# Optimization experiments

Measured on AMD Instinct MI355X. Metric: run time of the kernel, lower is better.

The kernel has to match this reference:

```python
import jax, jax.numpy as jnp
import numpy as np

P = 7    # pool size (hard-coded in module)
DS = 16  # downsample rate


def _hat_int(t):
    # antiderivative of the bilinear hat kernel max(0, 1-|t|)
    t = jnp.clip(t, -1.0, 1.0)
    return jnp.where(t < 0, 0.5 * (t + 1.0) ** 2, 1.0 - 0.5 * (1.0 - t) ** 2)


def _axis_weights(lo, hi, size):
    # Exact per-pixel integration weights for PrRoIPool along one axis.
    # lo, hi: [R] scaled roi coords. Returns W [R,P,size], bin width [R].
    bw = (hi - lo) / P
    starts = lo[:, None] + bw[:, None] * jnp.arange(P, dtype=lo.dtype)  # [R,P]
    ends = starts + bw[:, None]
    idx = jnp.arange(size, dtype=lo.dtype)
    W = _hat_int(ends[:, :, None] - idx) - _hat_int(starts[:, :, None] - idx)
    return W, bw


def prroi_pool(feat, rois):
    # Precise RoI pooling: exact integral of the bilinearly-interpolated feature
    # over each bin (separable -> two small matmuls). feat [C,H,W], rois [R,4].
    C, H, Wd = feat.shape
    s = 1.0 / DS
    Wx, bw = _axis_weights(rois[:, 0] * s, rois[:, 2] * s, Wd)
    Wy, bh = _axis_weights(rois[:, 1] * s, rois[:, 3] * s, H)
    pooled = jnp.einsum('chw,rph,rqw->rcpq', feat, Wy, Wx)  # [R,C,P,P]
    area = jnp.maximum(bw * bh, 1e-8)
    return pooled / area[:, None, None, None]


def intersection_map(box1, box2):
    # Fractional coverage of each PxP bin of box2's grid by box1 -> [N,1,P,P]
    bw = (box2[:, 2] - box2[:, 0]) / P
    bh = (box2[:, 3] - box2[:, 1]) / P
    gx0 = box2[:, 0, None] + bw[:, None] * jnp.arange(P)
    gy0 = box2[:, 1, None] + bh[:, None] * jnp.arange(P)
    ox = jnp.clip(jnp.minimum(gx0 + bw[:, None], box1[:, 2, None]) - jnp.maximum(gx0, box1[:, 0, None]), 0.0)
    oy = jnp.clip(jnp.minimum(gy0 + bh[:, None], box1[:, 3, None]) - jnp.maximum(gy0, box1[:, 1, None]), 0.0)
    frac = oy[:, :, None] * ox[:, None, :] / jnp.maximum(bw * bh, 1e-8)[:, None, None]
    return frac[:, None]


def conv1x1(x, W, b):
    # 1x1 conv as a channel matmul; x [...,C,H,W], W [D,C], b [D]
    return jnp.einsum('...chw,dc->...dhw', x, W) + b[:, None, None]


def setup_inputs() -> dict:
    key = jax.random.key(0)
    ks = jax.random.split(key, 12)
    B, C, Hf, Wf, n = 8, 256, 32, 32, 16
    D1 = D2 = 256
    inp = jax.random.normal(ks[0], (B, C, Hf, Wf), dtype=jnp.float32)
    N = B * n
    xy1 = jax.random.uniform(ks[1], (N, 2), dtype=jnp.float32) * 380.0
    wh = 40.0 + jax.random.uniform(ks[2], (N, 2), dtype=jnp.float32) * 90.0
    objects = jnp.concatenate([xy1, xy1 + wh], axis=-1)  # valid boxes inside 512x512
    objects_length = jnp.full((B,), n, dtype=jnp.int32)

    def kaiming(k, shape, fan_in):
        return jax.random.normal(k, shape, dtype=jnp.float32) * np.float32(np.sqrt(2.0 / fan_in))

    rin = C // 2 * 3 + 2 * D1
    return {
        'input': inp, 'objects': objects, 'objects_length': objects_length,
        'Wc': kaiming(ks[3], (C, C), C), 'bc': jnp.zeros((C,), jnp.float32),
        'Wr': kaiming(ks[4], (C // 2 * 3, C), C), 'br': jnp.zeros((C // 2 * 3,), jnp.float32),
        'Wof': kaiming(ks[5], (D1, 2 * C), 2 * C), 'bof': jnp.zeros((D1,), jnp.float32),
        'Wrf': kaiming(ks[6], (D2, rin), rin), 'brf': jnp.zeros((D2,), jnp.float32),
        'Wofc': kaiming(ks[7], (D1, D1 * P * P), D1 * P * P), 'bofc': jnp.zeros((D1,), jnp.float32),
        'Wrfc': kaiming(ks[8], (D2, D2 * P * P), D2 * P * P), 'brfc': jnp.zeros((D2,), jnp.float32),
    }


def reference(input, objects, objects_length, Wc, bc, Wr, br, Wof, bof, Wrf, brf, Wofc, bofc, Wrfc, brfc):
    B, C, H, Wd = input.shape
    n = objects.shape[0] // B  # uniform object count per image
    boxes = objects.reshape(B, n, 4)
    ctx_all = conv1x1(input, Wc, bc)           # [B,C,H,W]
    rel_all = conv1x1(input, Wr, br)           # [B,3C/2,H,W]
    img_box = jnp.array([0.0, 0.0, Wd * DS, H * DS], dtype=input.dtype)
    sub_id = jnp.repeat(jnp.arange(n), n)
    obj_id = jnp.tile(jnp.arange(n), n)

    def per_image(feat, ctx, rel, box):
        # context pooled over the full-image box is identical for all objects
        ctx_pool = prroi_pool(ctx, img_box[None])[0]                    # [C,P,P]
        x_c, y_c = jnp.split(ctx_pool, 2, axis=0)
        box_imap = jax.lax.stop_gradient(
            intersection_map(box, jnp.broadcast_to(img_box, (n, 4))))  # [n,1,P,P]
        obj_pool = prroi_pool(feat, box)                                # [n,C,P,P]
        obj_in = jnp.concatenate([
            obj_pool,
            jnp.broadcast_to(x_c, (n,) + x_c.shape),
            y_c[None] * box_imap], axis=1)                              # [n,2C,P,P]
        obj_feat = conv1x1(obj_in, Wof, bof)                            # [n,D1,P,P]

        sub_box, ob_box = box[sub_id], box[obj_id]                      # [n*n,4]
        union = jax.lax.stop_gradient(jnp.concatenate(
            [jnp.minimum(sub_box[:, :2], ob_box[:, :2]),
             jnp.maximum(sub_box[:, 2:], ob_box[:, 2:])], axis=-1))
        sub_imap = jax.lax.stop_gradient(intersection_map(sub_box, union))
        obj_imap = jax.lax.stop_gradient(intersection_map(ob_box, union))
        rel_pool = prroi_pool(rel, union)                               # [n*n,3C/2,P,P]
        xr, yr, zr = jnp.split(rel_pool, 3, axis=1)
        rel_in = jnp.concatenate([
            obj_feat[sub_id], obj_feat[obj_id],
            xr, yr * sub_imap, zr * obj_imap], axis=1)                  # [n*n,2D1+3C/2,P,P]
        rel_feat = conv1x1(rel_in, Wrf, brf)                            # [n*n,D2,P,P]

        o = jax.nn.relu(obj_feat).reshape(n, -1) @ Wofc.T + bofc
        o = o / jnp.linalg.norm(o, axis=-1, keepdims=True)
        r = jax.nn.relu(rel_feat).reshape(n * n, -1) @ Wrfc.T + brfc
        r = r / jnp.linalg.norm(r, axis=-1, keepdims=True)
        return o, r.reshape(n, n, -1)

    obj_out, rel_out = jax.vmap(per_image)(input, ctx_all, rel_all, boxes)
    return obj_out, rel_out
```

## Files before the change

### kernel.cpp

```cpp
#include <hip/hip_runtime.h>
#include <hip/hip_bf16.h>


#define Bimg 8
#define Cch 256
#define HW 1024
#define CREL 384
#define CCAT 640
#define KFC 12544
#define STS 236

typedef __hip_bfloat16 bf16;
typedef __attribute__((ext_vector_type(8))) short short8;
typedef __attribute__((ext_vector_type(4))) short short4_t;
typedef __attribute__((ext_vector_type(4))) float f32x4;

__device__ __forceinline__ float hat_int(float t) {
    t = fminf(1.f, fmaxf(-1.f, t));
    return (t < 0.f) ? 0.5f * (t + 1.f) * (t + 1.f) : 1.f - 0.5f * (1.f - t) * (1.f - t);
}
__device__ __forceinline__ float b2f(short s) {
    return __uint_as_float(((unsigned)(unsigned short)s) << 16);
}
__device__ __forceinline__ unsigned pack2bf(float a, float b) {
    bf16 ha = __float2bfloat16(a), hb = __float2bfloat16(b);
    return ((unsigned)(unsigned short)(*(short*)&hb) << 16) | (unsigned short)(*(short*)&ha);
}

__global__ void prep_k(const float* __restrict__ Wc, const float* __restrict__ bc,
                       const float* __restrict__ Wr, const float* __restrict__ br,
                       bf16* __restrict__ Wcat, float* __restrict__ bcat,
                       const float* __restrict__ Wof, bf16* __restrict__ wof16,
                       const float* __restrict__ Wrf, bf16* __restrict__ wasao16,
                       bf16* __restrict__ wrfxyz16) {
    int bid = blockIdx.x, tid = threadIdx.x;
    if (bid < 640) {
        int t = bid * 256 + tid;
        int d = t >> 8, c = t & 255;
        Wcat[t] = __float2bfloat16((d < 256) ? Wc[d * 256 + c] : Wr[(d - 256) * 256 + c]);
        if (t < CCAT) bcat[t] = (t < 256) ? bc[t] : br[t - 256];
    } else if (bid < 1152) {
        int t = (bid - 640) * 256 + tid;
        wof16[t] = __float2bfloat16(Wof[t]);
    } else if (bid < 1664) {
        int t = (bid - 1152) * 256 + tid;
        int m = t >> 8, k = t & 255;
        wasao16[t] = __float2bfloat16((m < 256) ? Wrf[m * 896 + k] : Wrf[(m - 256) * 896 + 256 + k]);
    } else {
        int t = (bid - 1664) * 256 + tid;
        int d = t / 384, k = t - d * 384;
        wrfxyz16[t] = __float2bfloat16(Wrf[d * 896 + 512 + k]);
    }
}
__global__ __launch_bounds__(256) void wfc_pack_k(const float* __restrict__ W, bf16* __restrict__ dst) {
    __shared__ float ld[64 * 50];
    int dout = blockIdx.y, d0 = blockIdx.x * 64;
    int tid = threadIdx.x;
    for (int e = tid; e < 64 * 49; e += 256) {
        int di = e / 49, pq = e - di * 49;
        ld[di * 50 + pq] = W[(size_t)dout * KFC + (d0 + di) * 49 + pq];
    }
    __syncthreads();
    for (int e = tid; e < 64 * 49; e += 256) {
        int pq = e >> 6, di = e & 63;
        if (pq < 49)
            dst[(size_t)dout * KFC + pq * 256 + d0 + di] = __float2bfloat16(ld[di * 50 + pq]);
    }
}

__global__ void axisw_k(const float* __restrict__ objects,
                        float* __restrict__ orec, float* __restrict__ urec,
                        float* __restrict__ crec, float* __restrict__ bimap) {
    int bid = blockIdx.x;
    float b0, b1, b2, b3;
    float* rec;
    const float *sbp = nullptr, *obp = nullptr;
    if (bid < 128) {
        b0 = objects[bid * 4]; b1 = objects[bid * 4 + 1];
        b2 = objects[bid * 4 + 2]; b3 = objects[bid * 4 + 3];
        rec = orec + (size_t)bid * 128;
    } else if (bid < 2176) {
        int u = bid - 128;
        int img = u >> 8, pair = u & 255, i = pair >> 4, j = pair & 15;
        sbp = objects + (img * 16 + i) * 4;
        obp = objects + (img * 16 + j) * 4;
        b0 = fminf(sbp[0], obp[0]); b1 = fminf(sbp[1], obp[1]);
        b2 = fmaxf(sbp[2], obp[2]); b3 = fmaxf(sbp[3], obp[3]);
        rec = urec + (size_t)(u) * 224;
    } else {
        b0 = 0.f; b1 = 0.f; b2 = 512.f; b3 = 512.f;
        rec = crec;
    }
    const float sc = 0.0625f;
    float lox = b0 * sc, bwx = (b2 * sc - lox) * (1.f / 7.f);
    float loy = b1 * sc, bwy = (b3 * sc - loy) * (1.f / 7.f);
    float ia = 1.f / fmaxf(bwx * bwy, 1e-8f);
    int tid = threadIdx.x;
    if (tid < 56) {
        int p = tid >> 3, k = tid & 7;
        {
            float st = loy + bwy * p, en = st + bwy;
            int h0 = min(max((int)floorf(st) - 1, 0), 24);
            rec[tid] = hat_int(en - (float)(h0 + k)) - hat_int(st - (float)(h0 + k));
            if (k == 0) ((int*)rec)[119 + p] = h0;
        }
        {
            float st = lox + bwx * p, en = st + bwx;
            int w0 = min(max((int)floorf(st) - 1, 0), 24);
            rec[56 + tid] = ia * (hat_int(en - (float)(w0 + k)) - hat_int(st - (float)(w0 + k)));
            if (k == 0) ((int*)rec)[112 + p] = w0;
        }
    }
    if (tid < 49) {
        int p = tid / 7, q = tid - p * 7;
        if (bid < 128) {
            float bw = 512.f / 7.f, bh = 512.f / 7.f;
            float gx0 = bw * q, gy0 = bh * p;
            float ox = fmaxf(fminf(gx0 + bw, b2) - fmaxf(gx0, b0), 0.f);
            float oy = fmaxf(fminf(gy0 + bh, b3) - fmaxf(gy0, b1), 0.f);
            bimap[bid * 49 + tid] = oy * ox / fmaxf(bw * bh, 1e-8f);
        } else if (bid < 2176) {
            float bw = (b2 - b0) * (1.f / 7.f), bh = (b3 - b1) * (1.f / 7.f);
            float gx0 = b0 + bw * q, gy0 = b1 + bh * p;
            float inv = 1.f / fmaxf(bw * bh, 1e-8f);
            float oxs = fmaxf(fminf(gx0 + bw, sbp[2]) - fmaxf(gx0, sbp[0]), 0.f);
            float oys = fmaxf(fminf(gy0 + bh, sbp[3]) - fmaxf(gy0, sbp[1]), 0.f);
            rec[126 + tid] = oys * oxs * inv;
            float oxo = fmaxf(fminf(gx0 + bw, obp[2]) - fmaxf(gx0, obp[0]), 0.f);
            float oyo = fmaxf(fminf(gy0 + bh, obp[3]) - fmaxf(gy0, obp[1]), 0.f);
            rec[175 + tid] = oyo * oxo * inv;
        }
    }
}

__global__ __launch_bounds__(256) void int_t_k(const float* __restrict__ input, bf16* __restrict__ intp) {
    __shared__ float st[64][65];
    int hw0 = blockIdx.x * 64, c0 = blockIdx.y * 64, b = blockIdx.z;
    int tid = threadIdx.x;
#pragma unroll
    for (int i = 0; i < 16; i++) {
        int e = tid + i * 256;
        int c = e >> 6, hw = e & 63;
        st[c][hw] = input[(size_t)b * 262144 + (size_t)(c0 + c) * 1024 + hw0 + hw];
    }
    __syncthreads();
#pragma unroll
    for (int i = 0; i < 16; i++) {
        int e = tid + i * 256;
        int hw = e >> 6, c = e & 63;
        intp[((size_t)b * 1024 + hw0 + hw) * 256 + c0 + c] = __float2bfloat16(st[c][hw]);
    }
}

__global__ __launch_bounds__(256) void mfma_gemm_k(
    const bf16* __restrict__ A, int lda,
    const bf16* __restrict__ BT, int ldbt, long zB,
    int Ktiles, int splitk, int mode,
    float* __restrict__ Cf, int Mtot, int Ntot,
    const float* __restrict__ bias,
    const bf16* __restrict__ ASAOT, int bimg0,
    bf16* __restrict__ Ct, int ldct, long zC, bf16* __restrict__ Ct2) {
    __shared__ float tr[32 * 132];
    const int tid = threadIdx.x;
    const int m0 = blockIdx.y * 128, n0 = blockIdx.x * 128;
    int z = blockIdx.z;
    int kz = 0, bimg = bimg0;
    if (mode == 1) { BT += (size_t)z * zB; Ct += (size_t)z * zC; bimg = bimg0 + z; }
    else kz = z;
    const int tp = (Ktiles + splitk - 1) / splitk;
    const int kt0 = kz * tp;
    const int kt1 = min(Ktiles, kt0 + tp);
    const int lane = tid & 63, wid = tid >> 6;
    const int wm = (wid >> 1) * 64, wn = (wid & 1) * 64;
    const int lrow = lane & 15, lk = (lane >> 4) * 8;
    f32x4 acc[4][4];
#pragma unroll
    for (int i = 0; i < 4; i++)
#pragma unroll
        for (int j = 0; j < 4; j++) acc[i][j] = (f32x4){0.f, 0.f, 0.f, 0.f};
    const bf16* pA = A + (size_t)(m0 + wm + lrow) * lda + lk;
    const bf16* pB = BT + (size_t)(n0 + wn + lrow) * ldbt + lk;
    short8 a_c[4], b_c[4];
    if (kt0 < kt1) {
#pragma unroll
        for (int f = 0; f < 4; f++) {
            a_c[f] = *(const short8*)(pA + (size_t)f * 16 * lda + (size_t)kt0 * 32);
            b_c[f] = *(const short8*)(pB + (size_t)f * 16 * ldbt + (size_t)kt0 * 32);
        }
    }
    for (int kt = kt0; kt < kt1; kt++) {
        short8 a_n[4], b_n[4];
        if (kt + 1 < kt1) {
#pragma unroll
            for (int f = 0; f < 4; f++) {
                a_n[f] = *(const short8*)(pA + (size_t)f * 16 * lda + (size_t)(kt + 1) * 32);
                b_n[f] = *(const short8*)(pB + (size_t)f * 16 * ldbt + (size_t)(kt + 1) * 32);
            }
        }
#pragma unroll
        for (int i = 0; i < 4; i++)
#pragma unroll
            for (int j = 0; j < 4; j++)
                acc[i][j] = __builtin_amdgcn_mfma_f32_16x16x32_bf16(a_c[i], b_c[j], acc[i][j], 0, 0, 0);
#pragma unroll
        for (int f = 0; f < 4; f++) { a_c[f] = a_n[f]; b_c[f] = b_n[f]; }
    }
    const int rbase = (lane >> 4) * 4, cf = lane & 15;
    if (mode == 5) {
#pragma unroll
        for (int i = 0; i < 4; i++)
#pragma unroll
            for (int reg = 0; reg < 4; reg++) {
                int m = m0 + wm + i * 16 + rbase + reg;
                float bv = bias[m];
#pragma unroll
                for (int j = 0; j < 4; j++) {
                    int n = n0 + wn + j * 16 + cf;
                    Ct[(size_t)m * ldct + n] = __float2bfloat16(acc[i][j][reg] + bv);
                }
            }
        return;
    }
#pragma unroll 1
    for (int ci = 0; ci < 4; ci++) {
        __syncthreads();
        if ((wid & 1) == (ci >> 1)) {
            int jj0 = (ci & 1) * 2;
#pragma unroll
            for (int jj = jj0; jj < jj0 + 2; jj++)
#pragma unroll
                for (int i = 0; i < 4; i++)
#pragma unroll
                    for (int reg = 0; reg < 4; reg++) {
                        int nl = (wn + jj * 16 + cf) - 32 * ci;
                        int ml = wm + i * 16 + rbase + reg;
                        tr[nl * 132 + ml] = acc[i][jj][reg];
                    }
        }
        __syncthreads();
        if (mode == 2) {
            float* P = Cf + (size_t)kz * Mtot * Ntot;
            for (int e = tid; e < 1024; e += 256) {
                int nl = e >> 5, mq = (e & 31) * 4;
                int n = n0 + 32 * ci + nl;
                *(f32x4*)&P[(size_t)n * Mtot + m0 + mq] = *(f32x4*)&tr[nl * 132 + mq];
            }
        } else if (mode == 3 || mode == 6) {
            for (int e = tid; e < 2048; e += 256) {
                int nl = e >> 6, mq = (e & 63) * 2;
                int n = n0 + 32 * ci + nl;
                int m = m0 + mq;
                float v0 = tr[nl * 132 + mq] + (bias ? bias[m] : 0.f);
                float v1 = tr[nl * 132 + mq + 1] + (bias ? bias[m + 1] : 0.f);
                *(unsigned*)&Ct[(size_t)n * ldct + m] = pack2bf(v0, v1);
                if (mode == 6) {
                    int r = n / 49, pq = n - r * 49;
                    *(unsigned*)&Ct2[(size_t)r * KFC + pq * 256 + m] =
                        pack2bf(fmaxf(v0, 0.f), fmaxf(v1, 0.f));
                }
            }
        } else {
            for (int e = tid; e < 2048; e += 256) {
                int nl = e >> 6, mq = (e & 63) * 2;
                int n = n0 + 32 * ci + nl;
                int m = m0 + mq;
                int r = n / 49, pq = n - r * 49;
                int ii = r >> 4, jj2 = r & 15;
                size_t abase = ((size_t)bimg * 784 + ii * 49 + pq) * 512;
                size_t obase = ((size_t)bimg * 784 + jj2 * 49 + pq) * 512 + 256;
                float v0 = tr[nl * 132 + mq] + bias[m]
                         + b2f(*(const short*)&ASAOT[abase + m])
                         + b2f(*(const short*)&ASAOT[obase + m]);
                float v1 = tr[nl * 132 + mq + 1] + bias[m + 1]
                         + b2f(*(const short*)&ASAOT[abase + m + 1])
                         + b2f(*(const short*)&ASAOT[obase + m + 1]);
                *(unsigned*)&Ct[(size_t)r * KFC + pq * 256 + m] =
                    pack2bf(fmaxf(v0, 0.f), fmaxf(v1, 0.f));
            }
        }
    }
}

__global__ __launch_bounds__(256) void objpool_k(
    const float* __restrict__ input, const float* __restrict__ orec,
    bf16* __restrict__ objint) {
    int cg = blockIdx.x;
    int b = blockIdx.y;
    __shared__ float sF[8192];
    __shared__ float sT[2][1888];
    __shared__ float wb[2][128];
    int tid = threadIdx.x;
    const float* feat = input + (size_t)b * (Cch * HW) + (size_t)cg * 8 * HW;
    for (int e4 = tid; e4 < 2048; e4 += 256)
        *(f32x4*)&sF[e4 * 4] = *(const f32x4*)&feat[e4 * 4];
    const float* rb = orec + (size_t)b * 16 * 128;
    if (tid < 126) wb[0][tid] = rb[tid];
    int t1v = tid + 256;
    int c0 = tid / 56, r0 = tid - c0 * 56, p0 = r0 >> 3, w40 = r0 & 7;
    int c1 = t1v / 56, r1 = t1v - c1 * 56, p1 = r1 >> 3, w41 = r1 & 7;
    bool has1 = (t1v < 448);
    int sf0 = c0 * 1024 + w40 * 4, st0 = c0 * STS + p0 * 32 + w40 * 4;
    int sf1 = c1 * 1024 + w41 * 4, st1 = c1 * STS + p1 * 32 + w41 * 4;
    int xpq0 = tid >> 3, xc = tid & 7;
    int xp0 = xpq0 / 7, xq0 = xpq0 - xp0 * 7;
    int xpq1 = xpq0 + 32;
    int xp1 = xpq1 / 7, xq1 = xpq1 - xp1 * 7;
    bool xv1 = (xpq1 < 49);
    __syncthreads();
    for (int r2 = 0; r2 < 16; r2++) {
        const float* wc_ = wb[r2 & 1];
        float* stbuf = sT[r2 & 1];
        float pre;
        bool pf = (r2 < 15) && (tid < 126);
        if (pf) pre = rb[(r2 + 1) * 128 + tid];
        {
            int h0 = ((const int*)wc_)[119 + p0];
            const f32x4* f = (const f32x4*)&sF[sf0 + h0 * 32];
            f32x4 wya = *(const f32x4*)&wc_[p0 * 8];
            f32x4 wyb = *(const f32x4*)&wc_[p0 * 8 + 4];
            f32x4 a = f[0] * wya[0] + f[8] * wya[1] + f[16] * wya[2] + f[24] * wya[3]
                    + f[32] * wyb[0] + f[40] * wyb[1] + f[48] * wyb[2] + f[56] * wyb[3];
            *(f32x4*)&stbuf[st0] = a;
        }
        if (has1) {
            int h0 = ((const int*)wc_)[119 + p1];
            const f32x4* f = (const f32x4*)&sF[sf1 + h0 * 32];
            f32x4 wya = *(const f32x4*)&wc_[p1 * 8];
            f32x4 wyb = *(const f32x4*)&wc_[p1 * 8 + 4];
            f32x4 a = f[0] * wya[0] + f[8] * wya[1] + f[16] * wya[2] + f[24] * wya[3]
                    + f[32] * wyb[0] + f[40] * wyb[1] + f[48] * wyb[2] + f[56] * wyb[3];
            *(f32x4*)&stbuf[st1] = a;
        }
        f32x4 xwa0 = *(const f32x4*)&wc_[56 + xq0 * 8];
        f32x4 xwb0 = *(const f32x4*)&wc_[56 + xq0 * 8 + 4];
        int w0i0 = ((const int*)wc_)[112 + xq0];
        f32x4 xwa1 = {0, 0, 0, 0}, xwb1 = {0, 0, 0, 0};
        int w0i1 = 0;
        if (xv1) {
            xwa1 = *(const f32x4*)&wc_[56 + xq1 * 8];
            xwb1 = *(const f32x4*)&wc_[56 + xq1 * 8 + 4];
            w0i1 = ((const int*)wc_)[112 + xq1];
        }
        if (pf) wb[1 - (r2 & 1)][tid] = pre;
        __syncthreads();
        {
            bf16* orow = objint + ((size_t)b * 784 + (size_t)r2 * 49) * 512 + cg * 8 + xc;
            {
                const float* t = &stbuf[xc * STS + xp0 * 32 + w0i0];
                float s = t[0] * xwa0[0] + t[1] * xwa0[1] + t[2] * xwa0[2] + t[3] * xwa0[3]
                        + t[4] * xwb0[0] + t[5] * xwb0[1] + t[6] * xwb0[2] + t[7] * xwb0[3];
                orow[(size_t)xpq0 * 512] = __float2bfloat16(s);
            }
            if (xv1) {
                const float* t = &stbuf[xc * STS + xp1 * 32 + w0i1];
                float s = t[0] * xwa1[0] + t[1] * xwa1[1] + t[2] * xwa1[2] + t[3] * xwa1[3]
                        + t[4] * xwb1[0] + t[5] * xwb1[1] + t[6] * xwb1[2] + t[7] * xwb1[3];
                orow[(size_t)xpq1 * 512] = __float2bfloat16(s);
            }
        }
    }
}

__global__ __launch_bounds__(256) void ctxobjin_k(
    const bf16* __restrict__ ctxrelb, const float* __restrict__ crec,
    const float* __restrict__ bimap, bf16* __restrict__ objint) {
    int cg = blockIdx.x;
    int b = blockIdx.y;
    __shared__ float sF[8192];
    __shared__ float sT[1888];
    __shared__ float wc_[128];
    __shared__ float sBI[784];
    int tid = threadIdx.x;
    for (int e4 = tid; e4 < 2048; e4 += 256) {
        short4_t v = *(const short4_t*)&ctxrelb[(size_t)(cg * 8 + (e4 >> 8)) * 8192 + b * 1024 + (e4 & 255) * 4];
        f32x4 fv = {b2f(v[0]), b2f(v[1]), b2f(v[2]), b2f(v[3])};
        *(f32x4*)&sF[e4 * 4] = fv;
    }
    if (tid < 126) wc_[tid] = crec[tid];
    for (int e = tid; e < 784; e += 256) sBI[e] = bimap[b * 784 + e];
    __syncthreads();
    for (int tt = tid; tt < 448; tt += 256) {
        int c = tt / 56, r = tt - c * 56, p = r >> 3, w4 = r & 7;
        int h0 = ((const int*)wc_)[119 + p];
        const f32x4* f = (const f32x4*)&sF[c * 1024 + w4 * 4 + h0 * 32];
        f32x4 wya = *(const f32x4*)&wc_[p * 8];
        f32x4 wyb = *(const f32x4*)&wc_[p * 8 + 4];
        f32x4 a = f[0] * wya[0] + f[8] * wya[1] + f[16] * wya[2] + f[24] * wya[3]
                + f[32] * wyb[0] + f[40] * wyb[1] + f[48] * wyb[2] + f[56] * wyb[3];
        *(f32x4*)&sT[c * STS + p * 32 + w4 * 4] = a;
    }
    __syncthreads();
    bool scale = (cg >= 16);
    for (int e = tid; e < 392; e += 256) {
        int pq = e >> 3, c = e & 7;
        int p = pq / 7, q = pq - p * 7;
        int w0i = ((const int*)wc_)[112 + q];
        const float* t = &sT[c * STS + p * 32 + w0i];
        const f32x4* wx4 = (const f32x4*)&wc_[56 + q * 8];
        f32x4 a = wx4[0], b2 = wx4[1];
        float s = t[0] * a[0] + t[1] * a[1] + t[2] * a[2] + t[3] * a[3]
                + t[4] * b2[0] + t[5] * b2[1] + t[6] * b2[2] + t[7] * b2[3];
        int j = cg * 8 + c;
        bf16* orow = objint + ((size_t)b * 784 + pq) * 512 + 256 + j;
#pragma unroll
        for (int r = 0; r < 16; r++) {
            float m = scale ? sBI[r * 49 + pq] : 1.f;
            orow[(size_t)r * 49 * 512] = __float2bfloat16(s * m);
        }
    }
}

__global__ __launch_bounds__(256) void relpool_k(
    const bf16* __restrict__ ctxrelb, const float* __restrict__ urec,
    bf16* __restrict__ mbt, int b0) {
    int cg = blockIdx.x;
    int rg = blockIdx.y;
    int zi = blockIdx.z;
    int b = b0 + zi;
    mbt += (size_t)zi * 4816896;
    __shared__ float sF[8192];
    __shared__ float sT[2][1888];
    __shared__ float wb[2][224];
    int tid = threadIdx.x;
    for (int e4 = tid; e4 < 2048; e4 += 256) {
        short4_t v = *(const short4_t*)&ctxrelb[(size_t)(256 + cg * 8 + (e4 >> 8)) * 8192 + b * 1024 + (e4 & 255) * 4];
        f32x4 fv = {b2f(v[0]), b2f(v[1]), b2f(v[2]), b2f(v[3])};
        *(f32x4*)&sF[e4 * 4] = fv;
    }
    const float* rb = urec + ((size_t)b * 256 + (size_t)rg * 16) * 224;
    if (tid < 224) wb[0][tid] = rb[tid];
    int t1v = tid + 256;
    int c0 = tid / 56, r0 = tid - c0 * 56, p0 = r0 >> 3, w40 = r0 & 7;
    int c1 = t1v / 56, r1 = t1v - c1 * 56, p1 = r1 >> 3, w41 = r1 & 7;
    bool has1 = (t1v < 448);
    int sf0 = c0 * 1024 + w40 * 4, st0 = c0 * STS + p0 * 32 + w40 * 4;
    int sf1 = c1 * 1024 + w41 * 4, st1 = c1 * STS + p1 * 32 + w41 * 4;
    int xpq0 = tid >> 3, xc = tid & 7;
    int xp0 = xpq0 / 7, xq0 = xpq0 - xp0 * 7;
    int xpq1 = xpq0 + 32;
    int xp1 = xpq1 / 7, xq1 = xpq1 - xp1 * 7;
    bool xv1 = (xpq1 < 49);
    int cglob = cg * 8 + xc;
    int mclass = (cglob >= 256) ? 2 : (cglob >= 128 ? 1 : 0);
    __syncthreads();
    for (int r2 = 0; r2 < 16; r2++) {
        const float* wc_ = wb[r2 & 1];
        float* stbuf = sT[r2 & 1];
        float pre;
        bool pf = (r2 < 15) && (tid < 224);
        if (pf) pre = rb[(r2 + 1) * 224 + tid];
        {
            int h0 = ((const int*)wc_)[119 + p0];
            const f32x4* f = (const f32x4*)&sF[sf0 + h0 * 32];
            f32x4 wya = *(const f32x4*)&wc_[p0 * 8];
            f32x4 wyb = *(const f32x4*)&wc_[p0 * 8 + 4];
            f32x4 a = f[0] * wya[0] + f[8] * wya[1] + f[16] * wya[2] + f[24] * wya[3]
                    + f[32] * wyb[0] + f[40] * wyb[1] + f[48] * wyb[2] + f[56] * wyb[3];
            *(f32x4*)&stbuf[st0] = a;
        }
        if (has1) {
            int h0 = ((const int*)wc_)[119 + p1];
            const f32x4* f = (const f32x4*)&sF[sf1 + h0 * 32];
            f32x4 wya = *(const f32x4*)&wc_[p1 * 8];
            f32x4 wyb = *(const f32x4*)&wc_[p1 * 8 + 4];
            f32x4 a = f[0] * wya[0] + f[8] * wya[1] + f[16] * wya[2] + f[24] * wya[3]
                    + f[32] * wyb[0] + f[40] * wyb[1] + f[48] * wyb[2] + f[56] * wyb[3];
            *(f32x4*)&stbuf[st1] = a;
        }
        f32x4 xwa0 = *(const f32x4*)&wc_[56 + xq0 * 8];
        f32x4 xwb0 = *(const f32x4*)&wc_[56 + xq0 * 8 + 4];
        int w0i0 = ((const int*)wc_)[112 + xq0];
        float mul0 = (mclass == 2) ? wc_[175 + xpq0] : (mclass == 1 ? wc_[126 + xpq0] : 1.f);
        f32x4 xwa1 = {0, 0, 0, 0}, xwb1 = {0, 0, 0, 0};
        int w0i1 = 0;
        float mul1 = 1.f;
        if (xv1) {
            xwa1 = *(const f32x4*)&wc_[56 + xq1 * 8];
            xwb1 = *(const f32x4*)&wc_[56 + xq1 * 8 + 4];
            w0i1 = ((const int*)wc_)[112 + xq1];
            mul1 = (mclass == 2) ? wc_[175 + xpq1] : (mclass == 1 ? wc_[126 + xpq1] : 1.f);
        }
        if (pf) wb[1 - (r2 & 1)][tid] = pre;
        __syncthreads();
        {
            int r = rg * 16 + r2;
            bf16* orow = mbt + (size_t)r * 49 * 384 + cglob;
            {
                const float* t = &stbuf[xc * STS + xp0 * 32 + w0i0];
                float s = t[0] * xwa0[0] + t[1] * xwa0[1] + t[2] * xwa0[2] + t[3] * xwa0[3]
                        + t[4] * xwb0[0] + t[5] * xwb0[1] + t[6] * xwb0[2] + t[7] * xwb0[3];
                orow[(size_t)xpq0 * 384] = __float2bfloat16(s * mul0);
            }
            if (xv1) {
                const float* t = &stbuf[xc * STS + xp1 * 32 + w0i1];
                float s = t[0] * xwa1[0] + t[1] * xwa1[1] + t[2] * xwa1[2] + t[3] * xwa1[3]
                        + t[4] * xwb1[0] + t[5] * xwb1[1] + t[6] * xwb1[2] + t[7] * xwb1[3];
                orow[(size_t)xpq1 * 384] = __float2bfloat16(s * mul1);
            }
        }
    }
}

__global__ void redns_k(const float* __restrict__ Pd, const float* __restrict__ bias,
                        float* __restrict__ out, int N, int splitk, long outBase) {
    int vec = blockIdx.x, m = threadIdx.x;
    float s = bias[m];
    for (int z = 0; z < splitk; z++) s += Pd[(size_t)z * 256 * N + (size_t)vec * 256 + m];
    float ss = s * s;
    for (int o = 32; o > 0; o >>= 1) ss += __shfl_down(ss, o, 64);
    __shared__ float red[4];
    if ((m & 63) == 0) red[m >> 6] = ss;
    __syncthreads();
    float tot = red[0] + red[1] + red[2] + red[3];
    out[outBase + (size_t)vec * 256 + m] = s / sqrtf(tot);
}

extern "C" void kernel_launch(void* const* d_in, const int* in_sizes, int n_in,
                              void* d_out, int out_size, void* d_ws, size_t ws_size,
                              hipStream_t stream) {
    const float* input = (const float*)d_in[0];
    const float* objects = (const float*)d_in[1];
    const float* Wc = (const float*)d_in[3];
    const float* bc = (const float*)d_in[4];
    const float* Wr = (const float*)d_in[5];
    const float* br = (const float*)d_in[6];
    const float* Wof = (const float*)d_in[7];
    const float* bof = (const float*)d_in[8];
    const float* Wrf = (const float*)d_in[9];
    const float* brf = (const float*)d_in[10];
    const float* Wofc = (const float*)d_in[11];
    const float* bofc = (const float*)d_in[12];
    const float* Wrfc = (const float*)d_in[13];
    const float* brfc = (const float*)d_in[14];
    float* out = (float*)d_out;

    float* w = (float*)d_ws;
    bf16* WCAT16   = (bf16*)(w + 0);
    float* BCAT    = w + 81920;
    bf16* CTXRELB  = (bf16*)(w + 82560);
    float* OREC    = w + 2704000;
    float* UREC    = w + 2720384;
    float* CREC    = w + 3179136;
    float* BIMAP   = w + 3179264;
    bf16* ASAOT16  = (bf16*)(w + 3185536);
    bf16* WRFXYZ16 = (bf16*)(w + 4791168);
    bf16* WRFC16   = (bf16*)(w + 4840320);
    float* OVL     = w + 6445952;
    bf16* INT16    = (bf16*)(OVL + 0);
    bf16* WOF16    = (bf16*)(OVL + 1048576);
    bf16* WASAO16  = (bf16*)(OVL + 1114112);
    bf16* WOFC16   = (bf16*)(OVL + 1179648);
    bf16* OBJINT   = (bf16*)(OVL + 2785280);
    bf16* OBJFT    = (bf16*)(OVL + 4390912);
    bf16* XOT      = (bf16*)(OVL + 5193728);
    float* OPART   = OVL + 5996544;
    bf16* MBT4     = (bf16*)(OVL + 0);
    float* RPART   = OVL + 0;
    bf16* XBT4     = (bf16*)(OVL + 9633792);

    prep_k<<<dim3(2048), 256, 0, stream>>>(Wc, bc, Wr, br, WCAT16, BCAT,
                                           Wof, WOF16, Wrf, WASAO16, WRFXYZ16);
    wfc_pack_k<<<dim3(4, 256), 256, 0, stream>>>(Wrfc, WRFC16);
    wfc_pack_k<<<dim3(4, 256), 256, 0, stream>>>(Wofc, WOFC16);
    axisw_k<<<dim3(2177), 64, 0, stream>>>(objects, OREC, UREC, CREC, BIMAP);
    int_t_k<<<dim3(16, 4, 8), 256, 0, stream>>>(input, INT16);
    mfma_gemm_k<<<dim3(64, 5, 1), 256, 0, stream>>>(WCAT16, 256, INT16, 256, 0L, 8, 1, 5,
                                                    nullptr, 640, 8192, BCAT,
                                                    nullptr, 0, CTXRELB, 8192, 0L, nullptr);
    objpool_k<<<dim3(32, 8), 256, 0, stream>>>(input, OREC, OBJINT);
    ctxobjin_k<<<dim3(32, 8), 256, 0, stream>>>(CTXRELB, CREC, BIMAP, OBJINT);
    mfma_gemm_k<<<dim3(49, 2, 1), 256, 0, stream>>>(WOF16, 512, OBJINT, 512, 0L, 16, 1, 6,
                                                    nullptr, 256, 6272, bof,
                                                    nullptr, 0, OBJFT, 256, 0L, XOT);
    mfma_gemm_k<<<dim3(49, 4, 1), 256, 0, stream>>>(WASAO16, 256, OBJFT, 256, 0L, 8, 1, 3,
                                                    nullptr, 512, 6272, nullptr,
                                                    nullptr, 0, ASAOT16, 512, 0L, nullptr);
    mfma_gemm_k<<<dim3(1, 2, 56), 256, 0, stream>>>(WOFC16, KFC, XOT, KFC, 0L, 392, 56, 2,
                                                    OPART, 256, 128, nullptr,
                                                    nullptr, 0, nullptr, 0, 0L, nullptr);
    redns_k<<<dim3(128), 256, 0, stream>>>(OPART, bofc, out, 128, 56, 0L);

    for (int g = 0; g < 2; g++) {
        int b0 = g * 4;
        relpool_k<<<dim3(48, 16, 4), 256, 0, stream>>>(CTXRELB, UREC, MBT4, b0);
        mfma_gemm_k<<<dim3(98, 2, 4), 256, 0, stream>>>(WRFXYZ16, 384, MBT4, 384, 4816896L,
                                                        12, 1, 1,
                                                        nullptr, 256, KFC, brf,
                                                        ASAOT16, b0, XBT4, 0, 3211264L, nullptr);
        mfma_gemm_k<<<dim3(8, 2, 24), 256, 0, stream>>>(WRFC16, KFC, XBT4, KFC, 0L, 392, 24, 2,
                                                        RPART, 256, 1024, nullptr,
                                                        nullptr, 0, nullptr, 0, 0L, nullptr);
        redns_k<<<dim3(1024), 256, 0, stream>>>(RPART, brfc, out, 1024, 24,
                                                32768L + (long)g * 262144L);
    }
}
```

Before: 708.0 us.

## Add 256x64 tile GEMM kernel for relation-path GEMMs covering full M

Adds a specialized GEMM kernel whose block covers all 256 output rows (four waves stacked along M) against a 64-wide N tile, and uses it for the two relation-path GEMMs. Each B tile is now loaded once instead of twice across two M-blocks, which cuts redundant reads of the large activation and FC operands. The mode-1 epilogue also writes eight bf16 values per store instead of two. The original GEMM loses its batched and mode-1 paths. The trade-off is less A-operand reuse per block (64 N columns instead of 128) and a different grid shape and occupancy.

```diff
diff --git a/kernel.cpp b/kernel.cpp
--- a/kernel.cpp
+++ b/kernel.cpp
@@ -154,19 +154,15 @@
 
 __global__ __launch_bounds__(256) void mfma_gemm_k(
     const bf16* __restrict__ A, int lda,
-    const bf16* __restrict__ BT, int ldbt, long zB,
+    const bf16* __restrict__ BT, int ldbt,
     int Ktiles, int splitk, int mode,
     float* __restrict__ Cf, int Mtot, int Ntot,
     const float* __restrict__ bias,
-    const bf16* __restrict__ ASAOT, int bimg0,
-    bf16* __restrict__ Ct, int ldct, long zC, bf16* __restrict__ Ct2) {
+    bf16* __restrict__ Ct, int ldct, bf16* __restrict__ Ct2) {
     __shared__ float tr[32 * 132];
     const int tid = threadIdx.x;
     const int m0 = blockIdx.y * 128, n0 = blockIdx.x * 128;
-    int z = blockIdx.z;
-    int kz = 0, bimg = bimg0;
-    if (mode == 1) { BT += (size_t)z * zB; Ct += (size_t)z * zC; bimg = bimg0 + z; }
-    else kz = z;
+    int kz = blockIdx.z;
     const int tp = (Ktiles + splitk - 1) / splitk;
     const int kt0 = kz * tp;
     const int kt1 = min(Ktiles, kt0 + tp);
@@ -245,7 +241,7 @@
                 int n = n0 + 32 * ci + nl;
                 *(f32x4*)&P[(size_t)n * Mtot + m0 + mq] = *(f32x4*)&tr[nl * 132 + mq];
             }
-        } else if (mode == 3 || mode == 6) {
+        } else {
             for (int e = tid; e < 2048; e += 256) {
                 int nl = e >> 6, mq = (e & 63) * 2;
                 int n = n0 + 32 * ci + nl;
@@ -259,23 +255,97 @@
                         pack2bf(fmaxf(v0, 0.f), fmaxf(v1, 0.f));
                 }
             }
+        }
+    }
+}
+
+__global__ __launch_bounds__(256) void mfma_gemm256_k(
+    const bf16* __restrict__ A, int lda,
+    const bf16* __restrict__ BT, int ldbt, long zB,
+    int Ktiles, int splitk, int mode,
+    float* __restrict__ Cf, int Ntot,
+    const float* __restrict__ bias,
+    const bf16* __restrict__ ASAOT, int bimg0,
+    bf16* __restrict__ Ct, long zC) {
+    __shared__ float tr[16 * 260];
+    const int tid = threadIdx.x;
+    const int n0 = blockIdx.x * 64;
+    int z = blockIdx.z;
+    int kz = 0, bimg = bimg0;
+    if (mode == 1) { BT += (size_t)z * zB; Ct += (size_t)z * zC; bimg = bimg0 + z; }
+    else kz = z;
+    const int tp = (Ktiles + splitk - 1) / splitk;
+    const int kt0 = kz * tp;
+    const int kt1 = min(Ktiles, kt0 + tp);
+    const int lane = tid & 63, wid = tid >> 6;
+    const int wm = wid * 64;
+    const int lrow = lane & 15, lk = (lane >> 4) * 8;
+    f32x4 acc[4][4];
+#pragma unroll
+    for (int i = 0; i < 4; i++)
+#pragma unroll
+        for (int j = 0; j < 4; j++) acc[i][j] = (f32x4){0.f, 0.f, 0.f, 0.f};
+    const bf16* pA = A + (size_t)(wm + lrow) * lda + lk;
+    const bf16* pB = BT + (size_t)(n0 + lrow) * ldbt + lk;
+    short8 a_c[4], b_c[4];
+    if (kt0 < kt1) {
+#pragma unroll
+        for (int f = 0; f < 4; f++) {
+            a_c[f] = *(const short8*)(pA + (size_t)f * 16 * lda + (size_t)kt0 * 32);
+            b_c[f] = *(const short8*)(pB + (size_t)f * 16 * ldbt + (size_t)kt0 * 32);
+        }
+    }
+    for (int kt = kt0; kt < kt1; kt++) {
+        short8 a_n[4], b_n[4];
+        if (kt + 1 < kt1) {
+#pragma unroll
+            for (int f = 0; f < 4; f++) {
+                a_n[f] = *(const short8*)(pA + (size_t)f * 16 * lda + (size_t)(kt + 1) * 32);
+                b_n[f] = *(const short8*)(pB + (size_t)f * 16 * ldbt + (size_t)(kt + 1) * 32);
+            }
+        }
+#pragma unroll
+        for (int i = 0; i < 4; i++)
+#pragma unroll
+            for (int j = 0; j < 4; j++)
+                acc[i][j] = __builtin_amdgcn_mfma_f32_16x16x32_bf16(a_c[i], b_c[j], acc[i][j], 0, 0, 0);
+#pragma unroll
+        for (int f = 0; f < 4; f++) { a_c[f] = a_n[f]; b_c[f] = b_n[f]; }
+    }
+    const int rbase = (lane >> 4) * 4, cf = lane & 15;
+#pragma unroll 1
+    for (int ci = 0; ci < 4; ci++) {
+        __syncthreads();
+#pragma unroll
+        for (int i = 0; i < 4; i++)
+#pragma unroll
+            for (int reg = 0; reg < 4; reg++)
+                tr[cf * 260 + wm + i * 16 + rbase + reg] = acc[i][ci][reg];
+        __syncthreads();
+        if (mode == 2) {
+            float* P = Cf + (size_t)kz * 256 * Ntot;
+            for (int e = tid; e < 1024; e += 256) {
+                int nl = e >> 6, mq = (e & 63) * 4;
+                int n = n0 + 16 * ci + nl;
+                *(f32x4*)&P[(size_t)n * 256 + mq] = *(f32x4*)&tr[nl * 260 + mq];
+            }
         } else {
-            for (int e = tid; e < 2048; e += 256) {
-                int nl = e >> 6, mq = (e & 63) * 2;
-                int n = n0 + 32 * ci + nl;
-                int m = m0 + mq;
+            for (int e = tid; e < 512; e += 256) {
+                int nl = e >> 5, mq = (e & 31) * 8;
+                int n = n0 + 16 * ci + nl;
                 int r = n / 49, pq = n - r * 49;
                 int ii = r >> 4, jj2 = r & 15;
-                size_t abase = ((size_t)bimg * 784 + ii * 49 + pq) * 512;
-                size_t obase = ((size_t)bimg * 784 + jj2 * 49 + pq) * 512 + 256;
-                float v0 = tr[nl * 132 + mq] + bias[m]
-                         + b2f(*(const short*)&ASAOT[abase + m])
-                         + b2f(*(const short*)&ASAOT[obase + m]);
-                float v1 = tr[nl * 132 + mq + 1] + bias[m + 1]
-                         + b2f(*(const short*)&ASAOT[abase + m + 1])
-                         + b2f(*(const short*)&ASAOT[obase + m + 1]);
-                *(unsigned*)&Ct[(size_t)r * KFC + pq * 256 + m] =
-                    pack2bf(fmaxf(v0, 0.f), fmaxf(v1, 0.f));
+                const bf16* as = &ASAOT[((size_t)bimg * 784 + ii * 49 + pq) * 512 + mq];
+                const bf16* ao = &ASAOT[((size_t)bimg * 784 + jj2 * 49 + pq) * 512 + 256 + mq];
+                short8 pk;
+#pragma unroll
+                for (int u = 0; u < 8; u++) {
+                    float v = tr[nl * 260 + mq + u] + bias[mq + u]
+                            + b2f(*(const short*)&as[u]) + b2f(*(const short*)&ao[u]);
+                    bf16 h = __float2bfloat16(fmaxf(v, 0.f));
+                    pk[u] = *(short*)&h;
+                }
+                *(short8*)&Ct[(size_t)r * KFC + pq * 256 + mq] = pk;
             }
         }
     }
@@ -564,32 +634,33 @@
     wfc_pack_k<<<dim3(4, 256), 256, 0, stream>>>(Wofc, WOFC16);
     axisw_k<<<dim3(2177), 64, 0, stream>>>(objects, OREC, UREC, CREC, BIMAP);
     int_t_k<<<dim3(16, 4, 8), 256, 0, stream>>>(input, INT16);
-    mfma_gemm_k<<<dim3(64, 5, 1), 256, 0, stream>>>(WCAT16, 256, INT16, 256, 0L, 8, 1, 5,
+    mfma_gemm_k<<<dim3(64, 5, 1), 256, 0, stream>>>(WCAT16, 256, INT16, 256, 8, 1, 5,
                                                     nullptr, 640, 8192, BCAT,
-                                                    nullptr, 0, CTXRELB, 8192, 0L, nullptr);
+                                                    CTXRELB, 8192, nullptr);
     objpool_k<<<dim3(32, 8), 256, 0, stream>>>(input, OREC, OBJINT);
     ctxobjin_k<<<dim3(32, 8), 256, 0, stream>>>(CTXRELB, CREC, BIMAP, OBJINT);
-    mfma_gemm_k<<<dim3(49, 2, 1), 256, 0, stream>>>(WOF16, 512, OBJINT, 512, 0L, 16, 1, 6,
+    mfma_gemm_k<<<dim3(49, 2, 1), 256, 0, stream>>>(WOF16, 512, OBJINT, 512, 16, 1, 6,
                                                     nullptr, 256, 6272, bof,
-                                                    nullptr, 0, OBJFT, 256, 0L, XOT);
-    mfma_gemm_k<<<dim3(49, 4, 1), 256, 0, stream>>>(WASAO16, 256, OBJFT, 256, 0L, 8, 1, 3,
+                                                    OBJFT, 256, XOT);
+    mfma_gemm_k<<<dim3(49, 4, 1), 256, 0, stream>>>(WASAO16, 256, OBJFT, 256, 8, 1, 3,
                                                     nullptr, 512, 6272, nullptr,
-                                                    nullptr, 0, ASAOT16, 512, 0L, nullptr);
-    mfma_gemm_k<<<dim3(1, 2, 56), 256, 0, stream>>>(WOFC16, KFC, XOT, KFC, 0L, 392, 56, 2,
+                                                    ASAOT16, 512, nullptr);
+    mfma_gemm_k<<<dim3(1, 2, 56), 256, 0, stream>>>(WOFC16, KFC, XOT, KFC, 392, 56, 2,
                                                     OPART, 256, 128, nullptr,
-                                                    nullptr, 0, nullptr, 0, 0L, nullptr);
+                                                    nullptr, 0, nullptr);
     redns_k<<<dim3(128), 256, 0, stream>>>(OPART, bofc, out, 128, 56, 0L);
 
     for (int g = 0; g < 2; g++) {
         int b0 = g * 4;
         relpool_k<<<dim3(48, 16, 4), 256, 0, stream>>>(CTXRELB, UREC, MBT4, b0);
-        mfma_gemm_k<<<dim3(98, 2, 4), 256, 0, stream>>>(WRFXYZ16, 384, MBT4, 384, 4816896L,
-                                                        12, 1, 1,
-                                                        nullptr, 256, KFC, brf,
-                                                        ASAOT16, b0, XBT4, 0, 3211264L, nullptr);
-        mfma_gemm_k<<<dim3(8, 2, 24), 256, 0, stream>>>(WRFC16, KFC, XBT4, KFC, 0L, 392, 24, 2,
-                                                        RPART, 256, 1024, nullptr,
-                                                        nullptr, 0, nullptr, 0, 0L, nullptr);
+        mfma_gemm256_k<<<dim3(196, 1, 4), 256, 0, stream>>>(WRFXYZ16, 384, MBT4, 384, 4816896L,
+                                                            12, 1, 1,
+                                                            nullptr, KFC, brf,
+                                                            ASAOT16, b0, XBT4, 3211264L);
+        mfma_gemm256_k<<<dim3(16, 1, 24), 256, 0, stream>>>(WRFC16, KFC, XBT4, KFC, 0L,
+                                                            392, 24, 2,
+                                                            RPART, 1024, nullptr,
+                                                            nullptr, 0, nullptr, 0L);
         redns_k<<<dim3(1024), 256, 0, stream>>>(RPART, brfc, out, 1024, 24,
                                                 32768L + (long)g * 262144L);
     }
```

Result: faster. 678.4 us (-4.2%).
